# Kernel optimization log

Hardware: AMD Instinct MI355X
Metric: run time of the kernel (lower is better)

Reference implementation:

```python
import jax, jax.numpy as jnp
import numpy as np

BANDWIDTH = 0.1
NUM_ITERS = 5


def setup_inputs() -> dict:
    key = jax.random.key(0)
    # image batch in [0,1], BCHW
    x = jax.random.uniform(key, (2, 3, 96, 96), dtype=jnp.float32)
    return {"x": x}


def reference(x):
    # Mean-shift filtering: each pixel feature y is iteratively moved to the
    # Gaussian-kernel weighted mean of ALL original pixel features:
    #   y_{t+1} = sum_j exp(-||y_t - x_j||^2 / (2 bw^2)) x_j / sum_j exp(...)
    B, C, H, W = x.shape
    N = H * W
    pts = x.reshape(B, C, N).transpose(0, 2, 1)  # [B, N, C] original points
    inv2bw2 = jnp.float32(1.0 / (2.0 * BANDWIDTH * BANDWIDTH))
    x_sq = jnp.sum(pts * pts, axis=-1)  # [B, N]

    def step(y, _):
        # squared pairwise distances via ||y||^2 + ||x||^2 - 2 y.x  -> [B, N, N]
        y_sq = jnp.sum(y * y, axis=-1)  # [B, N]
        d2 = y_sq[:, :, None] + x_sq[:, None, :] - 2.0 * jnp.einsum(
            'bnc,bmc->bnm', y, pts)
        w = jnp.exp(-jnp.maximum(d2, 0.0) * inv2bw2)  # Gaussian kernel weights
        num = jnp.einsum('bnm,bmc->bnc', w, pts)  # weighted sum of points
        den = jnp.sum(w, axis=-1, keepdims=True)  # normalizer (>= 1, self-weight)
        return num / den, None

    y, _ = jax.lax.scan(step, pts, None, length=NUM_ITERS)
    return y.transpose(0, 2, 1).reshape(B, C, H, W)
```

## Files before the change

kernel.cpp:

```cpp
#include <hip/hip_runtime.h>
#include <math.h>


#define NPTS   9216
#define NB     2
#define MSPLIT 12
#define SLICE  (NPTS / MSPLIT)
#define WSLICE (SLICE / 4)
#define NPB    128
#define NTILES (NPTS / NPB)
#define INV2BW2 50.0f
#define LOG2E   1.44269504088896340736f


__global__ __launch_bounds__(256) void ms_init(const float* __restrict__ x,
                                               float4* __restrict__ part,
                                               float s) {
    int gid = blockIdx.x * 256 + threadIdx.x;
    int b = gid / NPTS;
    int n = gid - b * NPTS;
    const float* xb = x + b * 3 * NPTS;
    float4 p0;
    p0.x = xb[n] * s;
    p0.y = xb[NPTS + n] * s;
    p0.z = xb[2 * NPTS + n] * s;
    p0.w = 1.0f;
    float4* dst = part + (size_t)gid * MSPLIT;
    dst[0] = p0;
    float4 z = make_float4(0.f, 0.f, 0.f, 0.f);
#pragma unroll
    for (int k = 1; k < MSPLIT; ++k) dst[k] = z;
}

__global__ __launch_bounds__(256) void ms_iter(const float* __restrict__ x,
                                               const float4* __restrict__ pin,
                                               float4* __restrict__ pout,
                                               float s) {
    __shared__ float4 buf[SLICE];

    const int tid  = threadIdx.x;
    const int lane = tid & 63;
    const int wv   = tid >> 6;
    const int k    = blockIdx.x % MSPLIT;
    const int tile = blockIdx.x / MSPLIT;
    const int b    = tile / NTILES;
    const int nt   = tile - b * NTILES;
    const int nbase = nt * NPB;
    const float* xb = x + b * 3 * NPTS;
    const int mbeg = k * SLICE;

    for (int i = tid; i < SLICE; i += 256) {
        int g = mbeg + i;
        float px = xb[g] * s;
        float py = xb[NPTS + g] * s;
        float pz = xb[2 * NPTS + g] * s;
        float4 p;
        p.x = px; p.y = py; p.z = pz;
        p.w = -fmaf(px, px, fmaf(py, py, pz * pz));
        buf[i] = p;
    }

    const float4* srcA = pin + (size_t)(b * NPTS + nbase + lane) * MSPLIT;
    const float4* srcB = srcA + (size_t)64 * MSPLIT;
    float nA0=0,nA1=0,nA2=0,dA=0, nB0=0,nB1=0,nB2=0,dB=0;
#pragma unroll
    for (int kk = 0; kk < MSPLIT; ++kk) {
        float4 a = srcA[kk];
        float4 c = srcB[kk];
        nA0+=a.x; nA1+=a.y; nA2+=a.z; dA+=a.w;
        nB0+=c.x; nB1+=c.y; nB2+=c.z; dB+=c.w;
    }
    const float invA = 1.0f / dA, invB = 1.0f / dB;
    const float yA0=nA0*invA, yA1=nA1*invA, yA2=nA2*invA;
    const float yB0=nB0*invB, yB1=nB1*invB, yB2=nB2*invB;
    const float mA0=2.f*yA0, mA1=2.f*yA1, mA2=2.f*yA2;
    const float mB0=2.f*yB0, mB1=2.f*yB1, mB2=2.f*yB2;
    const float cA = -fmaf(yA0,yA0,fmaf(yA1,yA1,yA2*yA2));
    const float cB = -fmaf(yB0,yB0,fmaf(yB1,yB1,yB2*yB2));

    __syncthreads();

    float a00=0,a01=0,a02=0,a03=0, a10=0,a11=0,a12=0,a13=0;
    const float4* pw = buf + wv * WSLICE;
#pragma unroll 4
    for (int i = 0; i < WSLICE; ++i) {
        float4 p = pw[i];
        float uA = fmaf(p.x, mA0, fmaf(p.y, mA1, fmaf(p.z, mA2, p.w + cA)));
        float uB = fmaf(p.x, mB0, fmaf(p.y, mB1, fmaf(p.z, mB2, p.w + cB)));
        float wA = __builtin_amdgcn_exp2f(uA);
        float wB = __builtin_amdgcn_exp2f(uB);
        a00 = fmaf(wA, p.x, a00); a01 = fmaf(wA, p.y, a01);
        a02 = fmaf(wA, p.z, a02); a03 += wA;
        a10 = fmaf(wB, p.x, a10); a11 = fmaf(wB, p.y, a11);
        a12 = fmaf(wB, p.z, a12); a13 += wB;
    }

    __syncthreads();
    buf[wv * NPB + lane]      = make_float4(a00, a01, a02, a03);
    buf[wv * NPB + 64 + lane] = make_float4(a10, a11, a12, a13);
    __syncthreads();
    if (tid < NPB) {
        float4 r0 = buf[tid];
        float4 r1 = buf[NPB + tid];
        float4 r2 = buf[2 * NPB + tid];
        float4 r3 = buf[3 * NPB + tid];
        float4 o;
        o.x = (r0.x + r1.x) + (r2.x + r3.x);
        o.y = (r0.y + r1.y) + (r2.y + r3.y);
        o.z = (r0.z + r1.z) + (r2.z + r3.z);
        o.w = (r0.w + r1.w) + (r2.w + r3.w);
        pout[(size_t)(b * NPTS + nbase + tid) * MSPLIT + k] = o;
    }
}

__global__ __launch_bounds__(256) void ms_pack(const float4* __restrict__ part,
                                               float* __restrict__ out,
                                               float invs) {
    int gid = blockIdx.x * 256 + threadIdx.x;
    int b = gid / NPTS;
    int n = gid - b * NPTS;
    const float4* src = part + (size_t)gid * MSPLIT;
    float n0 = 0.f, n1 = 0.f, n2 = 0.f, dn = 0.f;
#pragma unroll
    for (int kk = 0; kk < MSPLIT; ++kk) {
        float4 p = src[kk];
        n0 += p.x; n1 += p.y; n2 += p.z; dn += p.w;
    }
    float f = invs / dn;
    float* ob = out + b * 3 * NPTS;
    ob[n]            = n0 * f;
    ob[NPTS + n]     = n1 * f;
    ob[2 * NPTS + n] = n2 * f;
}

extern "C" void kernel_launch(void* const* d_in, const int* in_sizes, int n_in,
                              void* d_out, int out_size, void* d_ws, size_t ws_size,
                              hipStream_t stream) {
    const float* x = (const float*)d_in[0];
    float* out = (float*)d_out;
    const float s = sqrtf(INV2BW2 * LOG2E);

    float4* pa = (float4*)d_ws;
    float4* pb = pa + (size_t)NB * NPTS * MSPLIT;

    ms_init<<<NB * NPTS / 256, 256, 0, stream>>>(x, pa, s);
    float4* cur = pa;
    float4* nxt = pb;
    for (int it = 0; it < 5; ++it) {
        ms_iter<<<NB * NTILES * MSPLIT, 256, 0, stream>>>(x, cur, nxt, s);
        float4* t = cur; cur = nxt; nxt = t;
    }
    ms_pack<<<NB * NPTS / 256, 256, 0, stream>>>(cur, out, 1.0f / s);
}
```

Before: 290.2 us.

## Process four query points per thread and double the source-point split

Each thread now accumulates four query points instead of two, and the tile grows to 256 queries while the source split doubles to keep the grid size. Query parameters are computed once per thread and shared through LDS. The aim is to amortize each LDS point load over more exp/FMA work. In exchange the per-point partial buffer doubles, adding global traffic in the reduction, and register pressure rises.

```diff
diff --git a/kernel.cpp b/kernel.cpp
--- a/kernel.cpp
+++ b/kernel.cpp
@@ -4,10 +4,10 @@
 
 #define NPTS   9216
 #define NB     2
-#define MSPLIT 12
+#define MSPLIT 24
 #define SLICE  (NPTS / MSPLIT)
 #define WSLICE (SLICE / 4)
-#define NPB    128
+#define NPB    256
 #define NTILES (NPTS / NPB)
 #define INV2BW2 50.0f
 #define LOG2E   1.44269504088896340736f
@@ -36,7 +36,10 @@
                                                const float4* __restrict__ pin,
                                                float4* __restrict__ pout,
                                                float s) {
-    __shared__ float4 buf[SLICE];
+    __shared__ float4 smem[4 * NPB];
+    float4* const pts  = smem;
+    float4* const ypar = smem + SLICE;
+    float4* const red  = smem;
 
     const int tid  = threadIdx.x;
     const int lane = tid & 63;
@@ -57,53 +60,69 @@
         float4 p;
         p.x = px; p.y = py; p.z = pz;
         p.w = -fmaf(px, px, fmaf(py, py, pz * pz));
-        buf[i] = p;
+        pts[i] = p;
     }
 
-    const float4* srcA = pin + (size_t)(b * NPTS + nbase + lane) * MSPLIT;
-    const float4* srcB = srcA + (size_t)64 * MSPLIT;
-    float nA0=0,nA1=0,nA2=0,dA=0, nB0=0,nB1=0,nB2=0,dB=0;
+    {
+        const float4* src = pin + (size_t)(b * NPTS + nbase + tid) * MSPLIT;
+        float n0 = 0.f, n1 = 0.f, n2 = 0.f, dn = 0.f;
 #pragma unroll
-    for (int kk = 0; kk < MSPLIT; ++kk) {
-        float4 a = srcA[kk];
-        float4 c = srcB[kk];
-        nA0+=a.x; nA1+=a.y; nA2+=a.z; dA+=a.w;
-        nB0+=c.x; nB1+=c.y; nB2+=c.z; dB+=c.w;
+        for (int kk = 0; kk < MSPLIT; ++kk) {
+            float4 p = src[kk];
+            n0 += p.x; n1 += p.y; n2 += p.z; dn += p.w;
+        }
+        float inv = 1.0f / dn;
+        float y0 = n0 * inv, y1 = n1 * inv, y2 = n2 * inv;
+        float4 yp;
+        yp.x = 2.f * y0; yp.y = 2.f * y1; yp.z = 2.f * y2;
+        yp.w = -fmaf(y0, y0, fmaf(y1, y1, y2 * y2));
+        ypar[tid] = yp;
     }
-    const float invA = 1.0f / dA, invB = 1.0f / dB;
-    const float yA0=nA0*invA, yA1=nA1*invA, yA2=nA2*invA;
-    const float yB0=nB0*invB, yB1=nB1*invB, yB2=nB2*invB;
-    const float mA0=2.f*yA0, mA1=2.f*yA1, mA2=2.f*yA2;
-    const float mB0=2.f*yB0, mB1=2.f*yB1, mB2=2.f*yB2;
-    const float cA = -fmaf(yA0,yA0,fmaf(yA1,yA1,yA2*yA2));
-    const float cB = -fmaf(yB0,yB0,fmaf(yB1,yB1,yB2*yB2));
-
     __syncthreads();
 
-    float a00=0,a01=0,a02=0,a03=0, a10=0,a11=0,a12=0,a13=0;
-    const float4* pw = buf + wv * WSLICE;
+    float4 yp0 = ypar[lane];
+    float4 yp1 = ypar[lane + 64];
+    float4 yp2 = ypar[lane + 128];
+    float4 yp3 = ypar[lane + 192];
+
+    float4 a0 = make_float4(0.f, 0.f, 0.f, 0.f);
+    float4 a1 = make_float4(0.f, 0.f, 0.f, 0.f);
+    float4 a2 = make_float4(0.f, 0.f, 0.f, 0.f);
+    float4 a3 = make_float4(0.f, 0.f, 0.f, 0.f);
+
+    const float4* pw = pts + wv * WSLICE;
 #pragma unroll 4
     for (int i = 0; i < WSLICE; ++i) {
         float4 p = pw[i];
-        float uA = fmaf(p.x, mA0, fmaf(p.y, mA1, fmaf(p.z, mA2, p.w + cA)));
-        float uB = fmaf(p.x, mB0, fmaf(p.y, mB1, fmaf(p.z, mB2, p.w + cB)));
-        float wA = __builtin_amdgcn_exp2f(uA);
-        float wB = __builtin_amdgcn_exp2f(uB);
-        a00 = fmaf(wA, p.x, a00); a01 = fmaf(wA, p.y, a01);
-        a02 = fmaf(wA, p.z, a02); a03 += wA;
-        a10 = fmaf(wB, p.x, a10); a11 = fmaf(wB, p.y, a11);
-        a12 = fmaf(wB, p.z, a12); a13 += wB;
+        float u0 = fmaf(p.x, yp0.x, fmaf(p.y, yp0.y, fmaf(p.z, yp0.z, p.w + yp0.w)));
+        float u1 = fmaf(p.x, yp1.x, fmaf(p.y, yp1.y, fmaf(p.z, yp1.z, p.w + yp1.w)));
+        float u2 = fmaf(p.x, yp2.x, fmaf(p.y, yp2.y, fmaf(p.z, yp2.z, p.w + yp2.w)));
+        float u3 = fmaf(p.x, yp3.x, fmaf(p.y, yp3.y, fmaf(p.z, yp3.z, p.w + yp3.w)));
+        float w0 = __builtin_amdgcn_exp2f(u0);
+        float w1 = __builtin_amdgcn_exp2f(u1);
+        float w2 = __builtin_amdgcn_exp2f(u2);
+        float w3 = __builtin_amdgcn_exp2f(u3);
+        a0.x = fmaf(w0, p.x, a0.x); a0.y = fmaf(w0, p.y, a0.y);
+        a0.z = fmaf(w0, p.z, a0.z); a0.w += w0;
+        a1.x = fmaf(w1, p.x, a1.x); a1.y = fmaf(w1, p.y, a1.y);
+        a1.z = fmaf(w1, p.z, a1.z); a1.w += w1;
+        a2.x = fmaf(w2, p.x, a2.x); a2.y = fmaf(w2, p.y, a2.y);
+        a2.z = fmaf(w2, p.z, a2.z); a2.w += w2;
+        a3.x = fmaf(w3, p.x, a3.x); a3.y = fmaf(w3, p.y, a3.y);
+        a3.z = fmaf(w3, p.z, a3.z); a3.w += w3;
     }
 
     __syncthreads();
-    buf[wv * NPB + lane]      = make_float4(a00, a01, a02, a03);
-    buf[wv * NPB + 64 + lane] = make_float4(a10, a11, a12, a13);
+    red[wv * NPB + lane]       = a0;
+    red[wv * NPB + lane + 64]  = a1;
+    red[wv * NPB + lane + 128] = a2;
+    red[wv * NPB + lane + 192] = a3;
     __syncthreads();
-    if (tid < NPB) {
-        float4 r0 = buf[tid];
-        float4 r1 = buf[NPB + tid];
-        float4 r2 = buf[2 * NPB + tid];
-        float4 r3 = buf[3 * NPB + tid];
+    {
+        float4 r0 = red[tid];
+        float4 r1 = red[NPB + tid];
+        float4 r2 = red[2 * NPB + tid];
+        float4 r3 = red[3 * NPB + tid];
         float4 o;
         o.x = (r0.x + r1.x) + (r2.x + r3.x);
         o.y = (r0.y + r1.y) + (r2.y + r3.y);
```

Measured after the change: 311.3 us. 7.3% more time.
